# Kernel optimization log

Measured on AMD Instinct MI355X. Metric: run time of the kernel, lower is better.

Reference implementation:

```python
import jax, jax.numpy as jnp
import numpy as np

B = 32            # batch size
N = 100           # n_nodes (== MAX_N_NODES here)
MAXN = 100        # MAX_N_NODES
H = 256           # HIDDEN_DIM_FEATURES_EXTRACTOR
HA = 1024         # HIDDEN_DIM_ACTOR
HC = 512          # HIDDEN_DIM_CRITIC
K_ACTIVE = 5000   # exact number of active mask entries per batch element


def setup_inputs() -> dict:
    key = jax.random.key(0)
    ks = jax.random.split(key, 16)
    feat = jax.random.normal(ks[0], (B, N + 1, H), jnp.float32)
    # mask: exactly K_ACTIVE ones among N*N per batch row (dim == K for all rows)
    rng = np.random.default_rng(0)
    mask = np.zeros((B, N * N), np.float32)
    for i in range(B):
        mask[i, rng.choice(N * N, size=K_ACTIVE, replace=False)] = 1.0
    mask = jnp.asarray(mask).reshape(B, N, N)
    ext_mask = jnp.concatenate([jnp.zeros((B, 1, N), jnp.float32), mask], axis=1)  # [B, N+1, N]
    embedded_features = jnp.concatenate([feat, ext_mask], axis=2)  # [B, N+1, H+N]

    def lin(k, fi, fo):
        s = 1.0 / np.sqrt(fi)
        return (jax.random.uniform(k, (fi, fo), jnp.float32, -s, s),
                jax.random.uniform(jax.random.fold_in(k, 1), (fo,), jnp.float32, -s, s))

    aW1, ab1 = lin(ks[1], 3 * H, HA)
    aW2, ab2 = lin(ks[2], HA, HA)
    aW3, ab3 = lin(ks[3], HA, 1)
    cW1, cb1 = lin(ks[4], H, HC)
    cW2, cb2 = lin(ks[5], HC, HC)
    cW3, cb3 = lin(ks[6], HC, 1)
    return dict(embedded_features=embedded_features,
                aW1=aW1, ab1=ab1, aW2=aW2, ab2=ab2, aW3=aW3, ab3=ab3,
                cW1=cW1, cb1=cb1, cW2=cW2, cb2=cb2, cW3=cW3, cb3=cb3,
                K=K_ACTIVE)


def reference(embedded_features, aW1, ab1, aW2, ab2, aW3, ab3,
              cW1, cb1, cW2, cb2, cW3, cb3, K):
    # decompose features
    gn = embedded_features[:, :, :H]
    ext_mask = embedded_features[:, :, H:]
    g = gn[:, :1, :]                      # [B,1,H] graph embedding
    nodes = gn[:, 1:, :]                  # [B,N,H] node embeddings
    mask = ext_mask[:, 1:, :].reshape(B, -1)  # [B, N*N]

    # indexes of active pairs (stable top_k -> ascending indices among ones, like nonzero)
    _, idx = jax.lax.top_k(mask, K)       # [B,K] int32
    idx1 = idx // N
    idx2 = idx % N
    n1 = jnp.take_along_axis(nodes, idx1[:, :, None], axis=1)  # [B,K,H]
    n2 = jnp.take_along_axis(nodes, idx2[:, :, None], axis=1)  # [B,K,H]
    pairs = jnp.concatenate([jnp.broadcast_to(g, (B, K, H)), n1, n2], axis=-1)  # [B,K,3H]

    # actor MLP (tanh hidden activations)
    h = jnp.tanh(pairs @ aW1 + ab1)
    h = jnp.tanh(h @ aW2 + ab2)
    logits = h @ aW3 + ab3                # [B,K,1]
    pi = jax.nn.softmax(logits, axis=1)   # softmax over the K gathered pairs

    # scatter back into padded grid
    shaped = jnp.zeros((B, N * N), pi.dtype).at[jnp.arange(B)[:, None], idx].set(pi[..., 0])
    filled = jnp.zeros((B, MAXN, MAXN), pi.dtype).at[:, :N, :N].set(shaped.reshape(B, N, N))
    filled = filled.reshape(B, MAXN * MAXN)

    # critic MLP on graph embedding
    hv = jnp.tanh(g @ cW1 + cb1)
    hv = jnp.tanh(hv @ cW2 + cb2)
    value = hv @ cW3 + cb3                # [B,1,1]
    return filled, value
```

## Files before the change

### kernel.cpp

```cpp
#include <hip/hip_runtime.h>
#include <stdint.h>

#define AS1 __attribute__((address_space(1)))
#define AS3 __attribute__((address_space(3)))

typedef __bf16 bf16x8 __attribute__((ext_vector_type(8)));
typedef float  f32x4  __attribute__((ext_vector_type(4)));
typedef int    i32x4  __attribute__((ext_vector_type(4)));
typedef int    i32x8  __attribute__((ext_vector_type(8)));
typedef float  f32x16 __attribute__((ext_vector_type(16)));

__device__ __forceinline__ float tanh_fast(float x){
    float e = __expf(2.0f * x);
    return 1.0f - 2.0f * __builtin_amdgcn_rcpf(e + 1.0f);
}
__device__ __forceinline__ float tanh4_fast(float x){
    float e = __expf(2.0f * x);
    return fmaf(-8.0f, __builtin_amdgcn_rcpf(e + 1.0f), 4.0f);
}

__device__ __forceinline__ unsigned short f2bf(float f){
    unsigned int u = __float_as_uint(f);
    u = (u + 0x7fffu + ((u >> 16) & 1u)) >> 16;
    return (unsigned short)u;
}

template<int SEL>
__device__ __forceinline__ unsigned int pk4(unsigned int old, float a, float b){
#if defined(__has_builtin) && __has_builtin(__builtin_amdgcn_cvt_scalef32_pk_fp4_f32)
    return __builtin_amdgcn_cvt_scalef32_pk_fp4_f32(old, a, b, 1.0f, SEL);
#else
    float fa = fabsf(a), fb = fabsf(b);
    unsigned int ma = fa < 0.25f ? 0u : fa < 0.75f ? 1u : fa < 1.25f ? 2u :
                      fa < 1.75f ? 3u : fa < 2.5f  ? 4u : fa < 3.5f  ? 5u :
                      fa < 5.0f  ? 6u : 7u;
    unsigned int mb = fb < 0.25f ? 0u : fb < 0.75f ? 1u : fb < 1.25f ? 2u :
                      fb < 1.75f ? 3u : fb < 2.5f  ? 4u : fb < 3.5f  ? 5u :
                      fb < 5.0f  ? 6u : 7u;
    ma |= (a < 0.0f ? 8u : 0u); mb |= (b < 0.0f ? 8u : 0u);
    return old | ((ma | (mb << 4)) << (8 * SEL));
#endif
}

#define B2F(u, lo, hi) { lo = __uint_as_float((u) << 16); hi = __uint_as_float((u) & 0xffff0000u); }

__global__ __launch_bounds__(256) void k_stage1(
    const float* __restrict__ ef,  const float* __restrict__ aW1, const float* __restrict__ ab1,
    const float* __restrict__ aW2,
    const float* __restrict__ cW1, const float* __restrict__ cb1,
    const float* __restrict__ cW2, const float* __restrict__ cb2,
    const float* __restrict__ cW3, const float* __restrict__ cb3,
    int* __restrict__ pairs, unsigned char* __restrict__ w2b,
    unsigned short* __restrict__ P, float* __restrict__ out, int* __restrict__ qctr)
{
    int blk = blockIdx.x;
    int t = threadIdx.x;
    __shared__ __align__(16) unsigned short an[112 * 264];
    __shared__ float gsh[256], gpart[4][64];
    __shared__ int s_base, s_woff[4], s_wc[4];
    __shared__ float gs[256], h1[512], h2[512], wred[4];

    if (blk == 1024 && t == 0) qctr[0] = 0;

    if (blk < 1024){
        int cb = blk & 15, s = (blk >> 4) & 1, b = blk >> 5;
        for (int e = t; e < 25600; e += 256){
            int row = e >> 8, col = e & 255;
            an[row * 264 + col] = f2bf(ef[(size_t)b * 35956 + (size_t)(1 + row) * 356 + col]);
        }
        for (int e = t; e < 3168; e += 256) an[26400 + e] = 0;
        gsh[t] = ef[(size_t)b * 35956 + t];
        __syncthreads();

        if (s == 0){
            int cl = t & 63, q = t >> 6;
            const float* a1p = aW1 + (size_t)(q * 64) * 1024 + cb * 64 + cl;
            float p = 0.f;
            for (int i = 0; i < 64; ++i) p += gsh[q * 64 + i] * a1p[(size_t)i * 1024];
            gpart[q][cl] = p;
        }
        __syncthreads();

        int w = t >> 6, lane = t & 63, quad = lane >> 4, n = lane & 15;
        int c = cb * 64 + w * 16 + n;
        bf16x8 bfr[8];
        const float* wp = aW1 + (size_t)(256 + s * 256 + quad * 8) * 1024 + c;
#pragma unroll
        for (int kt = 0; kt < 8; ++kt){
            unsigned int ww[4];
#pragma unroll
            for (int jj = 0; jj < 4; ++jj){
                unsigned short lo = f2bf(wp[(size_t)(kt * 32 + 2 * jj) * 1024]);
                unsigned short hi = f2bf(wp[(size_t)(kt * 32 + 2 * jj + 1) * 1024]);
                ww[jj] = (unsigned int)lo | ((unsigned int)hi << 16);
            }
            uint4 pk = make_uint4(ww[0], ww[1], ww[2], ww[3]);
            bfr[kt] = *(bf16x8*)&pk;
        }
        f32x4 acc[7];
#pragma unroll
        for (int m = 0; m < 7; ++m){ f32x4 z = {0.f, 0.f, 0.f, 0.f}; acc[m] = z; }
#pragma unroll
        for (int kt = 0; kt < 8; ++kt){
#pragma unroll
            for (int m = 0; m < 7; ++m){
                const bf16x8* ap = (const bf16x8*)(an + (m * 16 + n) * 264 + kt * 32 + quad * 8);
                acc[m] = __builtin_amdgcn_mfma_f32_16x16x32_bf16(*ap, bfr[kt], acc[m], 0, 0, 0);
            }
        }
        int cw = w * 16 + n;
        float addv = (s == 0)
            ? (gpart[0][cw] + gpart[1][cw] + gpart[2][cw] + gpart[3][cw] + ab1[c]) : 0.0f;
        size_t base = (size_t)s * 3276800 + (size_t)b * 102400;
#pragma unroll
        for (int m = 0; m < 7; ++m){
            int r0 = m * 16 + quad * 4;
#pragma unroll
            for (int r = 0; r < 4; ++r){
                int row = r0 + r;
                if (row < 100) P[base + (size_t)row * 1024 + c] = f2bf(acc[m][r] + addv);
            }
        }
    } else if (blk < 1056){
        int b = blk - 1024;
        if (t == 0) s_base = 0;
        __syncthreads();
        int lane = t & 63, w = t >> 6;
        for (int ch = 0; ch < 40; ++ch){
            int pos = ch * 256 + t;
            bool valid = false;
            if (pos < 10000){
                int r = pos / 100, c = pos - (pos / 100) * 100;
                valid = ef[(size_t)b * 35956 + (size_t)(1 + r) * 356 + 256 + c] != 0.0f;
            }
            unsigned long long bal = __ballot(valid);
            if (lane == 0) s_wc[w] = __popcll(bal);
            __syncthreads();
            if (t == 0){
                int r = s_base;
                for (int q = 0; q < 4; ++q){ s_woff[q] = r; r += s_wc[q]; }
                s_base = r;
            }
            __syncthreads();
            if (valid){
                int rank = __popcll(bal & ((1ull << lane) - 1ull));
                int o = s_woff[w] + rank;
                if (o < 5000) pairs[b * 5000 + o] = pos;
            }
            __syncthreads();
        }
    } else if (blk < 1184){
        int tid = (blk - 1056) * 256 + t;
        int lane = tid & 63, kt = (tid >> 6) & 15, ct = tid >> 10;
        int lh = lane >> 5, n = lane & 31;
        const float* src = aW2 + (size_t)(kt * 64 + lh * 32) * 1024 + ct * 32 + n;
        unsigned int d[4] = {0u, 0u, 0u, 0u};
#pragma unroll
        for (int j = 0; j < 32; ++j){
            float a = src[(size_t)j * 1024] * 128.0f;
            float f = fabsf(a);
            unsigned int m = f < 0.25f ? 0u : f < 0.75f ? 1u : f < 1.25f ? 2u :
                             f < 1.75f ? 3u : f < 2.5f  ? 4u : f < 3.5f  ? 5u :
                             f < 5.0f  ? 6u : 7u;
            unsigned int nib = m | (a < 0.0f ? 8u : 0u);
            d[j >> 3] |= nib << (4 * (j & 7));
        }
        *(uint4*)(w2b + (size_t)(ct * 16 + kt) * 1024 + lane * 16) =
            make_uint4(d[0], d[1], d[2], d[3]);
    } else {
        int b = blk - 1184;
        gs[t] = ef[(size_t)b * 35956 + t];
        __syncthreads();
        for (int o = t; o < 512; o += 256){
            float a = cb1[o];
            for (int i = 0; i < 256; ++i) a += gs[i] * cW1[(size_t)i * 512 + o];
            h1[o] = tanh_fast(a);
        }
        __syncthreads();
        for (int o = t; o < 512; o += 256){
            float a = cb2[o];
            for (int i = 0; i < 512; ++i) a += h1[i] * cW2[(size_t)i * 512 + o];
            h2[o] = tanh_fast(a);
        }
        __syncthreads();
        float p = h2[t] * cW3[t] + h2[t + 256] * cW3[t + 256];
        for (int m = 32; m >= 1; m >>= 1) p += __shfl_xor(p, m);
        if ((t & 63) == 0) wred[t >> 6] = p;
        __syncthreads();
        if (t == 0) out[320000 + b] = wred[0] + wred[1] + wred[2] + wred[3] + cb3[0];
    }
}

__global__ __launch_bounds__(256, 3) void k_main(
    const int* __restrict__ pairs,
    const unsigned short* __restrict__ P1, const unsigned short* __restrict__ P2,
    const unsigned char* __restrict__ w2b, const float* __restrict__ ab2,
    const float* __restrict__ aW3, float* __restrict__ logits, int* __restrict__ qctr)
{
    __shared__ __align__(16) unsigned char wbuf[2][16384];
    __shared__ float saw3[1024], sab2[1024];
    __shared__ int s_tile;
    int t = threadIdx.x, w = t >> 6, lane = t & 63;
    int lrow = lane & 31, lh = lane >> 5;
    int soff = w * 4096 + lane * 16;

    for (int i = t; i < 1024; i += 256){ saw3[i] = aW3[i]; sab2[i] = ab2[i]; }

    for (;;){
        if (t == 0) s_tile = atomicAdd(qctr, 1);
        __syncthreads();
        int tt = s_tile;
        if (tt >= 1280) break;
        int b = tt / 40, tile = tt - b * 40;

        {
            const unsigned char* s = w2b + soff;
            unsigned char* d = &wbuf[0][0] + soff;
#pragma unroll
            for (int i = 0; i < 4; ++i)
                __builtin_amdgcn_global_load_lds((AS1 void*)(s + i * 1024),
                                                 (AS3 void*)(d + i * 1024), 16, 0, 0);
        }

        int grow = tile * 128 + w * 32 + lrow;
        int pidx = pairs[b * 5000 + (grow < 5000 ? grow : 4999)];
        int i1 = pidx / 100, i2 = pidx - i1 * 100;
        const uint4* pa = (const uint4*)(P1 + (((size_t)(b * 100 + i1)) << 10)) + lh * 4;
        const uint4* pb = (const uint4*)(P2 + (((size_t)(b * 100 + i2)) << 10)) + lh * 4;

        i32x4 af4[16];
#pragma unroll
        for (int kt = 0; kt < 16; ++kt){
            uint4 qa[4], qb[4];
#pragma unroll
            for (int j = 0; j < 4; ++j){ qa[j] = pa[kt * 8 + j]; qb[j] = pb[kt * 8 + j]; }
            unsigned int d[4];
#pragma unroll
            for (int j = 0; j < 4; ++j){
                float a0, a1, b0, b1;
                unsigned int dd = 0;
                B2F(qa[j].x, a0, a1); B2F(qb[j].x, b0, b1);
                dd = pk4<0>(dd, tanh4_fast(a0 + b0), tanh4_fast(a1 + b1));
                B2F(qa[j].y, a0, a1); B2F(qb[j].y, b0, b1);
                dd = pk4<1>(dd, tanh4_fast(a0 + b0), tanh4_fast(a1 + b1));
                B2F(qa[j].z, a0, a1); B2F(qb[j].z, b0, b1);
                dd = pk4<2>(dd, tanh4_fast(a0 + b0), tanh4_fast(a1 + b1));
                B2F(qa[j].w, a0, a1); B2F(qb[j].w, b0, b1);
                dd = pk4<3>(dd, tanh4_fast(a0 + b0), tanh4_fast(a1 + b1));
                d[j] = dd;
            }
            i32x4 f = {(int)d[0], (int)d[1], (int)d[2], (int)d[3]};
            af4[kt] = f;
        }

        float prt[16];
#pragma unroll
        for (int r = 0; r < 16; ++r) prt[r] = 0.f;
        f32x16 acc0, acc1;

        for (int ct = 0; ct < 32; ++ct){
            __syncthreads();
            if (ct < 31){
                const unsigned char* sp = w2b + (size_t)(ct + 1) * 16384 + soff;
                unsigned char* d = &wbuf[(ct + 1) & 1][0] + soff;
#pragma unroll
                for (int i = 0; i < 4; ++i)
                    __builtin_amdgcn_global_load_lds((AS1 void*)(sp + i * 1024),
                                                     (AS3 void*)(d + i * 1024), 16, 0, 0);
            }
#pragma unroll
            for (int r = 0; r < 16; ++r){ acc0[r] = 0.f; acc1[r] = 0.f; }
            const unsigned char* bb = &wbuf[ct & 1][0] + lane * 16;
#pragma unroll
            for (int j = 0; j < 8; ++j){
                uint4 q0 = *(const uint4*)(bb + (2 * j) * 1024);
                uint4 q1 = *(const uint4*)(bb + (2 * j + 1) * 1024);
                i32x4 a0 = af4[2 * j], a1 = af4[2 * j + 1];
                i32x8 aop0 = {a0[0], a0[1], a0[2], a0[3], a0[0], a0[1], a0[2], a0[3]};
                i32x8 aop1 = {a1[0], a1[1], a1[2], a1[3], a1[0], a1[1], a1[2], a1[3]};
                i32x8 b0 = {(int)q0.x, (int)q0.y, (int)q0.z, (int)q0.w, 0, 0, 0, 0};
                i32x8 b1 = {(int)q1.x, (int)q1.y, (int)q1.z, (int)q1.w, 0, 0, 0, 0};
                acc0 = __builtin_amdgcn_mfma_scale_f32_32x32x64_f8f6f4(
                           aop0, b0, acc0, 4, 4, 0, 0x7D7D7D7D, 0, 0x78787878);
                acc1 = __builtin_amdgcn_mfma_scale_f32_32x32x64_f8f6f4(
                           aop1, b1, acc1, 4, 4, 0, 0x7D7D7D7D, 0, 0x78787878);
            }
            int c = ct * 32 + lrow;
            float w3 = saw3[c], bias = sab2[c];
#pragma unroll
            for (int r = 0; r < 16; ++r)
                prt[r] += tanh_fast(acc0[r] + acc1[r] + bias) * w3;
        }

#pragma unroll
        for (int r = 0; r < 16; ++r){
            float v = prt[r];
            v += __shfl_xor(v, 1); v += __shfl_xor(v, 2); v += __shfl_xor(v, 4);
            v += __shfl_xor(v, 8); v += __shfl_xor(v, 16);
            if (lrow == 0){
                int row = (r & 3) + 8 * (r >> 2) + 4 * lh;
                int g = tile * 128 + w * 32 + row;
                if (g < 5000) logits[b * 5000 + g] = v;
            }
        }
    }
}

__global__ void k_soft(const float* __restrict__ logits, const int* __restrict__ pairs,
                       float* __restrict__ out){
    int b = blockIdx.x, t = threadIdx.x;
    __shared__ float red[4];
    __shared__ float bmS, bsS;
    float* ob = out + (size_t)b * 10000;
    for (int j = t; j < 10000; j += 256) ob[j] = 0.0f;
    const float* lg = logits + b * 5000;
    float m = -1e30f;
    for (int j = t; j < 5000; j += 256) m = fmaxf(m, lg[j]);
    for (int s = 32; s >= 1; s >>= 1) m = fmaxf(m, __shfl_xor(m, s));
    if ((t & 63) == 0) red[t >> 6] = m;
    __syncthreads();
    if (t == 0) bmS = fmaxf(fmaxf(red[0], red[1]), fmaxf(red[2], red[3]));
    __syncthreads();
    float mm = bmS;
    float s = 0.f;
    for (int j = t; j < 5000; j += 256) s += __expf(lg[j] - mm);
    for (int k = 32; k >= 1; k >>= 1) s += __shfl_xor(s, k);
    if ((t & 63) == 0) red[t >> 6] = s;
    __syncthreads();
    if (t == 0) bsS = 1.0f / (red[0] + red[1] + red[2] + red[3]);
    __syncthreads();
    float inv = bsS;
    for (int j = t; j < 5000; j += 256){
        int pos = pairs[b * 5000 + j];
        ob[pos] = __expf(lg[j] - mm) * inv;
    }
}

extern "C" void kernel_launch(void* const* d_in, const int* in_sizes, int n_in,
                              void* d_out, int out_size, void* d_ws, size_t ws_size,
                              hipStream_t stream) {
    (void)in_sizes; (void)n_in; (void)out_size; (void)ws_size;
    const float* ef  = (const float*)d_in[0];
    const float* aW1 = (const float*)d_in[1];
    const float* ab1 = (const float*)d_in[2];
    const float* aW2 = (const float*)d_in[3];
    const float* ab2 = (const float*)d_in[4];
    const float* aW3 = (const float*)d_in[5];
    const float* cW1 = (const float*)d_in[7];
    const float* cb1 = (const float*)d_in[8];
    const float* cW2 = (const float*)d_in[9];
    const float* cb2 = (const float*)d_in[10];
    const float* cW3 = (const float*)d_in[11];
    const float* cb3 = (const float*)d_in[12];
    float* out = (float*)d_out;
    char* ws = (char*)d_ws;
    int*   pairs  = (int*)(ws + 0);
    float* logits = (float*)(ws + 640000);
    unsigned short* P1 = (unsigned short*)(ws + 1411072);
    unsigned short* P2 = (unsigned short*)(ws + 7964672);
    unsigned char*  w2b = (unsigned char*)(ws + 14518272);
    int*   qctr   = (int*)(ws + 16615424);

    k_stage1<<<1216, 256, 0, stream>>>(ef, aW1, ab1, aW2, cW1, cb1, cW2, cb2, cW3, cb3,
                                       pairs, w2b, P1, out, qctr);
    k_main  <<<768,  256, 0, stream>>>(pairs, P1, P2, w2b, ab2, aW3, logits, qctr);
    k_soft  <<<32,   256, 0, stream>>>(logits, pairs, out);
}
```

Measured before the change: 318.5 us.

## Pretranspose W1 to bf16, split P GEMM kernel, restructure main MLP per-wave

```diff
diff --git a/kernel.cpp b/kernel.cpp
--- a/kernel.cpp
+++ b/kernel.cpp
@@ -1,8 +1,5 @@
 #include <hip/hip_runtime.h>
 #include <stdint.h>
-
-#define AS1 __attribute__((address_space(1)))
-#define AS3 __attribute__((address_space(3)))
 
 typedef __bf16 bf16x8 __attribute__((ext_vector_type(8)));
 typedef float  f32x4  __attribute__((ext_vector_type(4)));
@@ -45,84 +42,34 @@
 #define B2F(u, lo, hi) { lo = __uint_as_float((u) << 16); hi = __uint_as_float((u) & 0xffff0000u); }
 
 __global__ __launch_bounds__(256) void k_stage1(
-    const float* __restrict__ ef,  const float* __restrict__ aW1, const float* __restrict__ ab1,
+    const float* __restrict__ ef,  const float* __restrict__ aW1,
     const float* __restrict__ aW2,
     const float* __restrict__ cW1, const float* __restrict__ cb1,
     const float* __restrict__ cW2, const float* __restrict__ cb2,
     const float* __restrict__ cW3, const float* __restrict__ cb3,
-    int* __restrict__ pairs, unsigned char* __restrict__ w2b,
-    unsigned short* __restrict__ P, float* __restrict__ out, int* __restrict__ qctr)
+    int* __restrict__ pairs, unsigned short* __restrict__ w1t,
+    unsigned char* __restrict__ w2b, float* __restrict__ out, int* __restrict__ qctr)
 {
     int blk = blockIdx.x;
     int t = threadIdx.x;
-    __shared__ __align__(16) unsigned short an[112 * 264];
-    __shared__ float gsh[256], gpart[4][64];
     __shared__ int s_base, s_woff[4], s_wc[4];
     __shared__ float gs[256], h1[512], h2[512], wred[4];
 
-    if (blk == 1024 && t == 0) qctr[0] = 0;
-
-    if (blk < 1024){
-        int cb = blk & 15, s = (blk >> 4) & 1, b = blk >> 5;
-        for (int e = t; e < 25600; e += 256){
-            int row = e >> 8, col = e & 255;
-            an[row * 264 + col] = f2bf(ef[(size_t)b * 35956 + (size_t)(1 + row) * 356 + col]);
-        }
-        for (int e = t; e < 3168; e += 256) an[26400 + e] = 0;
-        gsh[t] = ef[(size_t)b * 35956 + t];
-        __syncthreads();
-
-        if (s == 0){
-            int cl = t & 63, q = t >> 6;
-            const float* a1p = aW1 + (size_t)(q * 64) * 1024 + cb * 64 + cl;
-            float p = 0.f;
-            for (int i = 0; i < 64; ++i) p += gsh[q * 64 + i] * a1p[(size_t)i * 1024];
-            gpart[q][cl] = p;
-        }
-        __syncthreads();
-
-        int w = t >> 6, lane = t & 63, quad = lane >> 4, n = lane & 15;
-        int c = cb * 64 + w * 16 + n;
-        bf16x8 bfr[8];
-        const float* wp = aW1 + (size_t)(256 + s * 256 + quad * 8) * 1024 + c;
-#pragma unroll
-        for (int kt = 0; kt < 8; ++kt){
-            unsigned int ww[4];
-#pragma unroll
-            for (int jj = 0; jj < 4; ++jj){
-                unsigned short lo = f2bf(wp[(size_t)(kt * 32 + 2 * jj) * 1024]);
-                unsigned short hi = f2bf(wp[(size_t)(kt * 32 + 2 * jj + 1) * 1024]);
-                ww[jj] = (unsigned int)lo | ((unsigned int)hi << 16);
-            }
-            uint4 pk = make_uint4(ww[0], ww[1], ww[2], ww[3]);
-            bfr[kt] = *(bf16x8*)&pk;
-        }
-        f32x4 acc[7];
-#pragma unroll
-        for (int m = 0; m < 7; ++m){ f32x4 z = {0.f, 0.f, 0.f, 0.f}; acc[m] = z; }
-#pragma unroll
-        for (int kt = 0; kt < 8; ++kt){
-#pragma unroll
-            for (int m = 0; m < 7; ++m){
-                const bf16x8* ap = (const bf16x8*)(an + (m * 16 + n) * 264 + kt * 32 + quad * 8);
-                acc[m] = __builtin_amdgcn_mfma_f32_16x16x32_bf16(*ap, bfr[kt], acc[m], 0, 0, 0);
-            }
-        }
-        int cw = w * 16 + n;
-        float addv = (s == 0)
-            ? (gpart[0][cw] + gpart[1][cw] + gpart[2][cw] + gpart[3][cw] + ab1[c]) : 0.0f;
-        size_t base = (size_t)s * 3276800 + (size_t)b * 102400;
-#pragma unroll
-        for (int m = 0; m < 7; ++m){
-            int r0 = m * 16 + quad * 4;
-#pragma unroll
-            for (int r = 0; r < 4; ++r){
-                int row = r0 + r;
-                if (row < 100) P[base + (size_t)row * 1024 + c] = f2bf(acc[m][r] + addv);
-            }
-        }
-    } else if (blk < 1056){
-        int b = blk - 1024;
+    if (blk == 256 && t == 0) qctr[0] = 0;
+
+    if (blk < 256){
+        int tid = blk * 256 + t;
+        int k8 = tid & 31, c = (tid >> 5) & 1023, s = tid >> 15;
+        const float* src = aW1 + (size_t)(256 + s * 256 + k8 * 8) * 1024 + c;
+        unsigned int* dst = (unsigned int*)(w1t + (size_t)tid * 8);
+#pragma unroll
+        for (int jj = 0; jj < 4; ++jj){
+            unsigned short lo = f2bf(src[(size_t)(2 * jj) * 1024]);
+            unsigned short hi = f2bf(src[(size_t)(2 * jj + 1) * 1024]);
+            dst[jj] = (unsigned int)lo | ((unsigned int)hi << 16);
+        }
+    } else if (blk < 288){
+        int b = blk - 256;
         if (t == 0) s_base = 0;
         __syncthreads();
         int lane = t & 63, w = t >> 6;
@@ -149,8 +96,8 @@
             }
             __syncthreads();
         }
-    } else if (blk < 1184){
-        int tid = (blk - 1056) * 256 + t;
+    } else if (blk < 416){
+        int tid = (blk - 288) * 256 + t;
         int lane = tid & 63, kt = (tid >> 6) & 15, ct = tid >> 10;
         int lh = lane >> 5, n = lane & 31;
         const float* src = aW2 + (size_t)(kt * 64 + lh * 32) * 1024 + ct * 32 + n;
@@ -167,8 +114,8 @@
         }
         *(uint4*)(w2b + (size_t)(ct * 16 + kt) * 1024 + lane * 16) =
             make_uint4(d[0], d[1], d[2], d[3]);
-    } else {
-        int b = blk - 1184;
+    } else if (blk < 448){
+        int b = blk - 416;
         gs[t] = ef[(size_t)b * 35956 + t];
         __syncthreads();
         for (int o = t; o < 512; o += 256){
@@ -188,119 +135,164 @@
         if ((t & 63) == 0) wred[t >> 6] = p;
         __syncthreads();
         if (t == 0) out[320000 + b] = wred[0] + wred[1] + wred[2] + wred[3] + cb3[0];
-    }
-}
-
-__global__ __launch_bounds__(256, 3) void k_main(
+    } else {
+        int i = (blk - 448) * 256 + t;
+        if (i < 80000) ((float4*)out)[i] = make_float4(0.f, 0.f, 0.f, 0.f);
+    }
+}
+
+__global__ __launch_bounds__(256) void k_p(const float* __restrict__ ef,
+        const unsigned short* __restrict__ w1t, unsigned short* __restrict__ P,
+        const float* __restrict__ aW1, const float* __restrict__ ab1){
+    __shared__ __align__(16) unsigned short an[112 * 264];
+    __shared__ float gsh[256], gpart[4][64];
+    int blk = blockIdx.x;
+    int cb = blk & 15, s = (blk >> 4) & 1, b = blk >> 5;
+    int t = threadIdx.x;
+    for (int e = t; e < 25600; e += 256){
+        int row = e >> 8, col = e & 255;
+        an[row * 264 + col] = f2bf(ef[(size_t)b * 35956 + (size_t)(1 + row) * 356 + col]);
+    }
+    for (int e = t; e < 3168; e += 256) an[26400 + e] = 0;
+    gsh[t] = ef[(size_t)b * 35956 + t];
+    __syncthreads();
+    if (s == 0){
+        int cl = t & 63, q = t >> 6;
+        const float* a1p = aW1 + (size_t)(q * 64) * 1024 + cb * 64 + cl;
+        float p = 0.f;
+        for (int i = 0; i < 64; ++i) p += gsh[q * 64 + i] * a1p[(size_t)i * 1024];
+        gpart[q][cl] = p;
+    }
+    __syncthreads();
+    int w = t >> 6, lane = t & 63, quad = lane >> 4, n = lane & 15;
+    int c = cb * 64 + w * 16 + n;
+    f32x4 acc[7];
+#pragma unroll
+    for (int m = 0; m < 7; ++m){ f32x4 z = {0.f, 0.f, 0.f, 0.f}; acc[m] = z; }
+    const bf16x8* wp = (const bf16x8*)(w1t + (size_t)(s * 1024 + c) * 256);
+#pragma unroll
+    for (int kt = 0; kt < 8; ++kt){
+        bf16x8 bfr = wp[kt * 4 + quad];
+#pragma unroll
+        for (int m = 0; m < 7; ++m){
+            const bf16x8* ap = (const bf16x8*)(an + (m * 16 + n) * 264 + kt * 32 + quad * 8);
+            acc[m] = __builtin_amdgcn_mfma_f32_16x16x32_bf16(*ap, bfr, acc[m], 0, 0, 0);
+        }
+    }
+    int cw = w * 16 + n;
+    float addv = (s == 0)
+        ? (gpart[0][cw] + gpart[1][cw] + gpart[2][cw] + gpart[3][cw] + ab1[c]) : 0.0f;
+    size_t base = (size_t)s * 3276800 + (size_t)b * 102400;
+#pragma unroll
+    for (int m = 0; m < 7; ++m){
+        int r0 = m * 16 + quad * 4;
+#pragma unroll
+        for (int r = 0; r < 4; ++r){
+            int row = r0 + r;
+            if (row < 100) P[base + (size_t)row * 1024 + c] = f2bf(acc[m][r] + addv);
+        }
+    }
+}
+
+__device__ __forceinline__ void build_af4(const uint4* __restrict__ pa,
+                                          const uint4* __restrict__ pb, i32x4* af){
+#pragma unroll
+    for (int kt = 0; kt < 16; ++kt){
+        uint4 qa[4], qb[4];
+#pragma unroll
+        for (int j = 0; j < 4; ++j){ qa[j] = pa[kt * 8 + j]; qb[j] = pb[kt * 8 + j]; }
+        unsigned int d[4];
+#pragma unroll
+        for (int j = 0; j < 4; ++j){
+            float a0, a1, b0, b1;
+            unsigned int dd = 0;
+            B2F(qa[j].x, a0, a1); B2F(qb[j].x, b0, b1);
+            dd = pk4<0>(dd, tanh4_fast(a0 + b0), tanh4_fast(a1 + b1));
+            B2F(qa[j].y, a0, a1); B2F(qb[j].y, b0, b1);
+            dd = pk4<1>(dd, tanh4_fast(a0 + b0), tanh4_fast(a1 + b1));
+            B2F(qa[j].z, a0, a1); B2F(qb[j].z, b0, b1);
+            dd = pk4<2>(dd, tanh4_fast(a0 + b0), tanh4_fast(a1 + b1));
+            B2F(qa[j].w, a0, a1); B2F(qb[j].w, b0, b1);
+            dd = pk4<3>(dd, tanh4_fast(a0 + b0), tanh4_fast(a1 + b1));
+            d[j] = dd;
+        }
+        i32x4 f = {(int)d[0], (int)d[1], (int)d[2], (int)d[3]};
+        af[kt] = f;
+    }
+}
+
+__device__ __forceinline__ i32x8 lo4(i32x4 a){
+    return __builtin_shufflevector(a, a, 0, 1, 2, 3, -1, -1, -1, -1);
+}
+
+__global__ __launch_bounds__(256, 2) void k_main(
     const int* __restrict__ pairs,
     const unsigned short* __restrict__ P1, const unsigned short* __restrict__ P2,
     const unsigned char* __restrict__ w2b, const float* __restrict__ ab2,
     const float* __restrict__ aW3, float* __restrict__ logits, int* __restrict__ qctr)
 {
-    __shared__ __align__(16) unsigned char wbuf[2][16384];
-    __shared__ float saw3[1024], sab2[1024];
-    __shared__ int s_tile;
-    int t = threadIdx.x, w = t >> 6, lane = t & 63;
+    int t = threadIdx.x, lane = t & 63;
     int lrow = lane & 31, lh = lane >> 5;
-    int soff = w * 4096 + lane * 16;
-
-    for (int i = t; i < 1024; i += 256){ saw3[i] = aW3[i]; sab2[i] = ab2[i]; }
+    const unsigned char* wb = w2b + lane * 16;
 
     for (;;){
-        if (t == 0) s_tile = atomicAdd(qctr, 1);
-        __syncthreads();
-        int tt = s_tile;
-        if (tt >= 1280) break;
-        int b = tt / 40, tile = tt - b * 40;
-
-        {
-            const unsigned char* s = w2b + soff;
-            unsigned char* d = &wbuf[0][0] + soff;
-#pragma unroll
-            for (int i = 0; i < 4; ++i)
-                __builtin_amdgcn_global_load_lds((AS1 void*)(s + i * 1024),
-                                                 (AS3 void*)(d + i * 1024), 16, 0, 0);
-        }
-
-        int grow = tile * 128 + w * 32 + lrow;
-        int pidx = pairs[b * 5000 + (grow < 5000 ? grow : 4999)];
-        int i1 = pidx / 100, i2 = pidx - i1 * 100;
-        const uint4* pa = (const uint4*)(P1 + (((size_t)(b * 100 + i1)) << 10)) + lh * 4;
-        const uint4* pb = (const uint4*)(P2 + (((size_t)(b * 100 + i2)) << 10)) + lh * 4;
-
-        i32x4 af4[16];
-#pragma unroll
-        for (int kt = 0; kt < 16; ++kt){
-            uint4 qa[4], qb[4];
-#pragma unroll
-            for (int j = 0; j < 4; ++j){ qa[j] = pa[kt * 8 + j]; qb[j] = pb[kt * 8 + j]; }
-            unsigned int d[4];
-#pragma unroll
-            for (int j = 0; j < 4; ++j){
-                float a0, a1, b0, b1;
-                unsigned int dd = 0;
-                B2F(qa[j].x, a0, a1); B2F(qb[j].x, b0, b1);
-                dd = pk4<0>(dd, tanh4_fast(a0 + b0), tanh4_fast(a1 + b1));
-                B2F(qa[j].y, a0, a1); B2F(qb[j].y, b0, b1);
-                dd = pk4<1>(dd, tanh4_fast(a0 + b0), tanh4_fast(a1 + b1));
-                B2F(qa[j].z, a0, a1); B2F(qb[j].z, b0, b1);
-                dd = pk4<2>(dd, tanh4_fast(a0 + b0), tanh4_fast(a1 + b1));
-                B2F(qa[j].w, a0, a1); B2F(qb[j].w, b0, b1);
-                dd = pk4<3>(dd, tanh4_fast(a0 + b0), tanh4_fast(a1 + b1));
-                d[j] = dd;
-            }
-            i32x4 f = {(int)d[0], (int)d[1], (int)d[2], (int)d[3]};
-            af4[kt] = f;
-        }
-
-        float prt[16];
-#pragma unroll
-        for (int r = 0; r < 16; ++r) prt[r] = 0.f;
+        int u = 0;
+        if (lane == 0) u = atomicAdd(qctr, 1);
+        u = __shfl(u, 0);
+        if (u >= 2528) break;
+        int b = u / 79, r0 = (u - b * 79) * 64;
+
+        int g0 = r0 + lrow, g1 = r0 + 32 + lrow;
+        int pidx0 = pairs[b * 5000 + (g0 < 5000 ? g0 : 4999)];
+        int pidx1 = pairs[b * 5000 + (g1 < 5000 ? g1 : 4999)];
+        int i10 = pidx0 / 100, i20 = pidx0 - i10 * 100;
+        int i11 = pidx1 / 100, i21 = pidx1 - i11 * 100;
+
+        i32x4 afa[16], afb[16];
+        build_af4((const uint4*)(P1 + (((size_t)(b * 100 + i10)) << 10)) + lh * 4,
+                  (const uint4*)(P2 + (((size_t)(b * 100 + i20)) << 10)) + lh * 4, afa);
+        build_af4((const uint4*)(P1 + (((size_t)(b * 100 + i11)) << 10)) + lh * 4,
+                  (const uint4*)(P2 + (((size_t)(b * 100 + i21)) << 10)) + lh * 4, afb);
+
+        float prt0[16], prt1[16];
+#pragma unroll
+        for (int r = 0; r < 16; ++r){ prt0[r] = 0.f; prt1[r] = 0.f; }
         f32x16 acc0, acc1;
 
         for (int ct = 0; ct < 32; ++ct){
-            __syncthreads();
-            if (ct < 31){
-                const unsigned char* sp = w2b + (size_t)(ct + 1) * 16384 + soff;
-                unsigned char* d = &wbuf[(ct + 1) & 1][0] + soff;
-#pragma unroll
-                for (int i = 0; i < 4; ++i)
-                    __builtin_amdgcn_global_load_lds((AS1 void*)(sp + i * 1024),
-                                                     (AS3 void*)(d + i * 1024), 16, 0, 0);
-            }
 #pragma unroll
             for (int r = 0; r < 16; ++r){ acc0[r] = 0.f; acc1[r] = 0.f; }
-            const unsigned char* bb = &wbuf[ct & 1][0] + lane * 16;
-#pragma unroll
-            for (int j = 0; j < 8; ++j){
-                uint4 q0 = *(const uint4*)(bb + (2 * j) * 1024);
-                uint4 q1 = *(const uint4*)(bb + (2 * j + 1) * 1024);
-                i32x4 a0 = af4[2 * j], a1 = af4[2 * j + 1];
-                i32x8 aop0 = {a0[0], a0[1], a0[2], a0[3], a0[0], a0[1], a0[2], a0[3]};
-                i32x8 aop1 = {a1[0], a1[1], a1[2], a1[3], a1[0], a1[1], a1[2], a1[3]};
-                i32x8 b0 = {(int)q0.x, (int)q0.y, (int)q0.z, (int)q0.w, 0, 0, 0, 0};
-                i32x8 b1 = {(int)q1.x, (int)q1.y, (int)q1.z, (int)q1.w, 0, 0, 0, 0};
+            const unsigned char* bs = wb + (size_t)ct * 16384;
+#pragma unroll
+            for (int kt = 0; kt < 16; ++kt){
+                uint4 q = *(const uint4*)(bs + kt * 1024);
+                i32x8 bop = {(int)q.x, (int)q.y, (int)q.z, (int)q.w, 0, 0, 0, 0};
                 acc0 = __builtin_amdgcn_mfma_scale_f32_32x32x64_f8f6f4(
-                           aop0, b0, acc0, 4, 4, 0, 0x7D7D7D7D, 0, 0x78787878);
+                           lo4(afa[kt]), bop, acc0, 4, 4, 0, 0x7D7D7D7D, 0, 0x78787878);
                 acc1 = __builtin_amdgcn_mfma_scale_f32_32x32x64_f8f6f4(
-                           aop1, b1, acc1, 4, 4, 0, 0x7D7D7D7D, 0, 0x78787878);
+                           lo4(afb[kt]), bop, acc1, 4, 4, 0, 0x7D7D7D7D, 0, 0x78787878);
             }
             int c = ct * 32 + lrow;
-            float w3 = saw3[c], bias = sab2[c];
-#pragma unroll
-            for (int r = 0; r < 16; ++r)
-                prt[r] += tanh_fast(acc0[r] + acc1[r] + bias) * w3;
+            float w3 = aW3[c], bias = ab2[c];
+#pragma unroll
+            for (int r = 0; r < 16; ++r){
+                prt0[r] += tanh_fast(acc0[r] + bias) * w3;
+                prt1[r] += tanh_fast(acc1[r] + bias) * w3;
+            }
         }
 
 #pragma unroll
         for (int r = 0; r < 16; ++r){
-            float v = prt[r];
-            v += __shfl_xor(v, 1); v += __shfl_xor(v, 2); v += __shfl_xor(v, 4);
-            v += __shfl_xor(v, 8); v += __shfl_xor(v, 16);
+            float v0 = prt0[r], v1 = prt1[r];
+            v0 += __shfl_xor(v0, 1); v0 += __shfl_xor(v0, 2); v0 += __shfl_xor(v0, 4);
+            v0 += __shfl_xor(v0, 8); v0 += __shfl_xor(v0, 16);
+            v1 += __shfl_xor(v1, 1); v1 += __shfl_xor(v1, 2); v1 += __shfl_xor(v1, 4);
+            v1 += __shfl_xor(v1, 8); v1 += __shfl_xor(v1, 16);
             if (lrow == 0){
                 int row = (r & 3) + 8 * (r >> 2) + 4 * lh;
-                int g = tile * 128 + w * 32 + row;
-                if (g < 5000) logits[b * 5000 + g] = v;
+                int ga = r0 + row, gb2 = r0 + 32 + row;
+                if (ga  < 5000) logits[b * 5000 + ga]  = v0;
+                if (gb2 < 5000) logits[b * 5000 + gb2] = v1;
             }
         }
     }
@@ -312,7 +304,6 @@
     __shared__ float red[4];
     __shared__ float bmS, bsS;
     float* ob = out + (size_t)b * 10000;
-    for (int j = t; j < 10000; j += 256) ob[j] = 0.0f;
     const float* lg = logits + b * 5000;
     float m = -1e30f;
     for (int j = t; j < 5000; j += 256) m = fmaxf(m, lg[j]);
@@ -359,10 +350,12 @@
     unsigned short* P1 = (unsigned short*)(ws + 1411072);
     unsigned short* P2 = (unsigned short*)(ws + 7964672);
     unsigned char*  w2b = (unsigned char*)(ws + 14518272);
+    unsigned short* w1t = (unsigned short*)(ws + 15566848);
     int*   qctr   = (int*)(ws + 16615424);
 
-    k_stage1<<<1216, 256, 0, stream>>>(ef, aW1, ab1, aW2, cW1, cb1, cW2, cb2, cW3, cb3,
-                                       pairs, w2b, P1, out, qctr);
-    k_main  <<<768,  256, 0, stream>>>(pairs, P1, P2, w2b, ab2, aW3, logits, qctr);
+    k_stage1<<<761,  256, 0, stream>>>(ef, aW1, aW2, cW1, cb1, cW2, cb2, cW3, cb3,
+                                       pairs, w1t, w2b, out, qctr);
+    k_p     <<<1024, 256, 0, stream>>>(ef, w1t, P1, aW1, ab1);
+    k_main  <<<512,  256, 0, stream>>>(pairs, P1, P2, w2b, ab2, aW3, logits, qctr);
     k_soft  <<<32,   256, 0, stream>>>(logits, pairs, out);
 }
```

Result: slower. 400.3 us (+25.7%).
